# Performance work log

Hardware: AMD Instinct MI355X
Metric: run time of the kernel (lower is better)

## Reference

```python
import jax, jax.numpy as jnp
import numpy as np

N, IN_FEAT, OUT_FEAT = 16384, 1024, 4096


def setup_inputs() -> dict:
    key = jax.random.key(0)
    k_x, k_m, k_w, k_b = jax.random.split(key, 4)
    x = jax.random.normal(k_x, (N, IN_FEAT), dtype=jnp.float32)
    amask = jax.random.randint(k_m, (N,), 0, 2, dtype=jnp.int32)
    # nn.Linear(in_feat, out_feat): weight [out, in], bias [out]
    W = jax.random.normal(k_w, (OUT_FEAT, IN_FEAT), dtype=jnp.float32) * (1.0 / np.sqrt(IN_FEAT))
    b = jax.random.normal(k_b, (OUT_FEAT,), dtype=jnp.float32) * 0.001
    return {"x": x, "amask": amask, "W": W, "b": b}


def reference(x, amask, W, b):
    # Torch code gathers rows where amask != 0, applies linear (+identity act),
    # and scatters results back into a zero [N, out_feat] tensor. Equivalent
    # dense-math (jit-friendly, no data-dependent shapes): compute the linear
    # on all rows and zero out unmasked rows. Same output values.
    y = jnp.einsum('ni,oi->no', x, W) + b  # [N, out_feat]
    keep = (amask != 0)[:, None]
    return jnp.where(keep, y, jnp.zeros((), dtype=x.dtype))
```

## Files before the change

### kernel.cpp

```cpp
#include <hip/hip_runtime.h>
#include <hip/hip_bf16.h>
#include <stdint.h>

#define N_ROWS 16384
#define K_DIM  1024
#define N_OUT  4096

typedef __attribute__((ext_vector_type(8))) short short8;
typedef __attribute__((ext_vector_type(4))) float f32x4;
typedef __attribute__((ext_vector_type(4))) __bf16 bf16x4;

__global__ __launch_bounds__(1024) void scan_kernel(const int* __restrict__ amask,
                                                    int* __restrict__ idx,
                                                    int* __restrict__ zidx,
                                                    int* __restrict__ count) {
    __shared__ int sc[1024];
    const int t = threadIdx.x;
    const int base = t * 16;
    int mk[16];
#pragma unroll
    for (int g = 0; g < 4; ++g) {
        int4 m4 = reinterpret_cast<const int4*>(amask + base)[g];
        mk[g*4+0] = m4.x; mk[g*4+1] = m4.y; mk[g*4+2] = m4.z; mk[g*4+3] = m4.w;
    }
    int c = 0;
#pragma unroll
    for (int i = 0; i < 16; ++i) c += (mk[i] != 0) ? 1 : 0;
    int v = c;
    sc[t] = v;
    __syncthreads();
    for (int off = 1; off < 1024; off <<= 1) {
        int u = (t >= off) ? sc[t - off] : 0;
        __syncthreads();
        v += u; sc[t] = v;
        __syncthreads();
    }
    int b  = v - c;
    int zb = base - b;
#pragma unroll
    for (int i = 0; i < 16; ++i) {
        int r = base + i;
        if (mk[i] != 0) idx[b++] = r; else zidx[zb++] = r;
    }
    if (t == 1023) count[0] = v;
}

__global__ __launch_bounds__(256) void cvtw_gather_kernel(
    const float* __restrict__ W, const float* __restrict__ x,
    const int* __restrict__ idx, const int* __restrict__ count,
    __bf16* __restrict__ wb, __bf16* __restrict__ xb) {
    const int t = threadIdx.x;
    if (blockIdx.x < 256) {
        const int base = blockIdx.x * 4096 + t;
#pragma unroll
        for (int it = 0; it < 16; ++it) {
            const int i = base + it * 256;
            float4 v = reinterpret_cast<const float4*>(W)[i];
            bf16x4 o;
            o[0] = (__bf16)v.x; o[1] = (__bf16)v.y; o[2] = (__bf16)v.z; o[3] = (__bf16)v.w;
            reinterpret_cast<bf16x4*>(wb)[i] = o;
        }
        return;
    }
    const int cnt = count[0];
    for (int j = blockIdx.x - 256; j < cnt; j += 2048) {
        const int row = idx[j];
        float4 v = reinterpret_cast<const float4*>(x + (size_t)row * K_DIM)[t];
        bf16x4 o;
        o[0] = (__bf16)v.x; o[1] = (__bf16)v.y; o[2] = (__bf16)v.z; o[3] = (__bf16)v.w;
        reinterpret_cast<bf16x4*>(xb + (size_t)j * K_DIM)[t] = o;
    }
}


#define GLL(SRC, DSTOFF)                                                       \
    __builtin_amdgcn_global_load_lds(                                          \
        (const __attribute__((address_space(1))) void*)(SRC),                  \
        (__attribute__((address_space(3))) void*)(ldsc + (DSTOFF)), 16, 0, 0)

__global__ __launch_bounds__(256) void gemm_kernel(
    const __bf16* __restrict__ A,
    const __bf16* __restrict__ B,
    const float*  __restrict__ bias,
    const int*    __restrict__ idx,
    const int*    __restrict__ zidx,
    const int*    __restrict__ count,
    float*        __restrict__ out)
{
    __shared__ short lds_all[16384];

    const int cnt = count[0];
    const int aT  = (cnt + 127) >> 7;
    const int tn  = blockIdx.x & 31;
    const int tm  = blockIdx.x >> 5;
    const int t   = threadIdx.x;

    if (tm >= aT) {
        const int ntriv = 4096 - aT * 32;
        const int tr    = blockIdx.x - aT * 32;
        const int nz    = N_ROWS - cnt;
        const float4 zf = make_float4(0.f, 0.f, 0.f, 0.f);
        for (int i = tr; i < nz; i += ntriv) {
            const int row = zidx[i];
            float4* p = reinterpret_cast<float4*>(out + (size_t)row * N_OUT);
#pragma unroll
            for (int u = 0; u < 4; ++u)
                p[u * 256 + t] = zf;
        }
        return;
    }

    const int l  = t & 63;
    const int w  = t >> 6;
    const int wm = w >> 1;
    const int wn = w & 1;

    const int m0 = tm * 128;
    const int n0 = tn * 128;

    const int srow = t >> 3;
    const int sk   = (t & 7) * 8;
    const __bf16* pA = A + (size_t)(m0 + srow) * K_DIM + sk;
    const __bf16* pB = B + (size_t)(n0 + srow) * K_DIM + sk;
    char* ldsc = (char*)lds_all;

    const int lr  = l & 15;
    const int lqb = (l >> 4) * 16;

    f32x4 acc[4][4] = {};

    for (int k0 = 0; k0 < K_DIM; k0 += 64) {
#pragma unroll
        for (int p = 0; p < 4; ++p) {
            GLL(pA + k0 + (size_t)(p * 32) * K_DIM, p * 4096 + t * 16);
            GLL(pB + k0 + (size_t)(p * 32) * K_DIM, 16384 + p * 4096 + t * 16);
        }
        __syncthreads();

#pragma unroll
        for (int s = 0; s < 2; ++s) {
            short8 af[4], bf[4];
#pragma unroll
            for (int mi = 0; mi < 4; ++mi)
                af[mi] = *(const short8*)((char*)lds_all +
                         (wm*64 + mi*16 + lr) * 128 + s * 64 + lqb);
#pragma unroll
            for (int ni = 0; ni < 4; ++ni)
                bf[ni] = *(const short8*)((char*)lds_all + 16384 +
                         (wn*64 + ni*16 + lr) * 128 + s * 64 + lqb);

#pragma unroll
            for (int mi = 0; mi < 4; ++mi)
#pragma unroll
                for (int ni = 0; ni < 4; ++ni)
                    acc[mi][ni] = __builtin_amdgcn_mfma_f32_16x16x32_bf16(
                        af[mi], bf[ni], acc[mi][ni], 0, 0, 0);
        }
        __syncthreads();
    }

    const int lq = l >> 4;
    float bv[4];
#pragma unroll
    for (int ni = 0; ni < 4; ++ni) bv[ni] = bias[n0 + wn*64 + ni*16 + lr];

#pragma unroll
    for (int mi = 0; mi < 4; ++mi) {
        const int slot0 = m0 + wm*64 + mi*16 + lq*4;
        int rowid[4]; bool val[4];
#pragma unroll
        for (int r = 0; r < 4; ++r) {
            const int s = slot0 + r;
            val[r] = (s < cnt);
            rowid[r] = val[r] ? idx[s] : 0;
        }
#pragma unroll
        for (int ni = 0; ni < 4; ++ni) {
            const int cc = n0 + wn*64 + ni*16 + lr;
#pragma unroll
            for (int r = 0; r < 4; ++r)
                if (val[r]) out[(size_t)rowid[r] * N_OUT + cc] = acc[mi][ni][r] + bv[ni];
        }
    }
}

__global__ void naive_kernel(const float* __restrict__ x, const float* __restrict__ W,
                             const float* __restrict__ bias, const int* __restrict__ amask,
                             float* __restrict__ out) {
    int c = blockIdx.x * blockDim.x + threadIdx.x;
    int r = blockIdx.y;
    if (c >= N_OUT) return;
    if (amask[r] == 0) { out[(size_t)r * N_OUT + c] = 0.0f; return; }
    const float* xr = x + (size_t)r * K_DIM;
    const float* wr = W + (size_t)c * K_DIM;
    float s = 0.0f;
    for (int k = 0; k < K_DIM; ++k) s += xr[k] * wr[k];
    out[(size_t)r * N_OUT + c] = s + bias[c];
}

extern "C" void kernel_launch(void* const* d_in, const int* in_sizes, int n_in,
                              void* d_out, int out_size, void* d_ws, size_t ws_size,
                              hipStream_t stream) {
    const float* x     = (const float*)d_in[0];
    const int*   amask = (const int*)d_in[1];
    const float* W     = (const float*)d_in[2];
    const float* bias  = (const float*)d_in[3];
    float*       out   = (float*)d_out;

    const size_t xb_bytes = (size_t)N_ROWS * K_DIM * 2;
    const size_t wb_bytes = (size_t)N_OUT  * K_DIM * 2;
    const size_t idx_bytes = (size_t)N_ROWS * 4;
    const size_t need = xb_bytes + wb_bytes + 2 * idx_bytes + 256;

    if (ws_size < need) {
        dim3 g((N_OUT + 255) / 256, N_ROWS);
        naive_kernel<<<g, 256, 0, stream>>>(x, W, bias, amask, out);
        return;
    }

    __bf16* xb   = (__bf16*)d_ws;
    __bf16* wb   = (__bf16*)((char*)d_ws + xb_bytes);
    int*    idx  = (int*)((char*)d_ws + xb_bytes + wb_bytes);
    int*    zidx = idx + N_ROWS;
    int*    cnt  = zidx + N_ROWS;

    scan_kernel<<<1, 1024, 0, stream>>>(amask, idx, zidx, cnt);
    cvtw_gather_kernel<<<2304, 256, 0, stream>>>(W, x, idx, cnt, wb, xb);
    gemm_kernel<<<4096, 256, 0, stream>>>(xb, wb, bias, idx, zidx, cnt, out);
}
```

Baseline: 181.7 us.

## Shrink GEMM K-tile to 32 and move zero-row writes into heavy blocks

Halves the K step per iteration (64 to 32), cutting LDS use from 32KB to 16KB so more blocks can be resident per CU, at the cost of twice as many barriers and load rounds. The zero-filling of unmasked output rows is moved from the idle trailing blocks into the tail of the GEMM blocks, which now write those rows after their epilogue. Trailing blocks exit immediately unless no rows are active. This changes how the zero-store traffic overlaps with GEMM compute, and each GEMM block now carries some extra store work.

Result: faster. 153.7 us (-15.4%).

```diff
diff --git a/kernel.cpp b/kernel.cpp
--- a/kernel.cpp
+++ b/kernel.cpp
@@ -87,25 +87,25 @@
     const int*    __restrict__ count,
     float*        __restrict__ out)
 {
-    __shared__ short lds_all[16384];
+    __shared__ short lds_all[8192];
 
     const int cnt = count[0];
     const int aT  = (cnt + 127) >> 7;
     const int tn  = blockIdx.x & 31;
     const int tm  = blockIdx.x >> 5;
     const int t   = threadIdx.x;
+    const int nz  = N_ROWS - cnt;
+    const float4 zf = make_float4(0.f, 0.f, 0.f, 0.f);
 
     if (tm >= aT) {
-        const int ntriv = 4096 - aT * 32;
-        const int tr    = blockIdx.x - aT * 32;
-        const int nz    = N_ROWS - cnt;
-        const float4 zf = make_float4(0.f, 0.f, 0.f, 0.f);
-        for (int i = tr; i < nz; i += ntriv) {
-            const int row = zidx[i];
-            float4* p = reinterpret_cast<float4*>(out + (size_t)row * N_OUT);
-#pragma unroll
-            for (int u = 0; u < 4; ++u)
-                p[u * 256 + t] = zf;
+        if (aT == 0) {
+            for (int i = blockIdx.x; i < nz; i += 4096) {
+                const int row = zidx[i];
+                float4* p = reinterpret_cast<float4*>(out + (size_t)row * N_OUT);
+#pragma unroll
+                for (int u = 0; u < 4; ++u)
+                    p[u * 256 + t] = zf;
+            }
         }
         return;
     }
@@ -118,44 +118,40 @@
     const int m0 = tm * 128;
     const int n0 = tn * 128;
 
-    const int srow = t >> 3;
-    const int sk   = (t & 7) * 8;
-    const __bf16* pA = A + (size_t)(m0 + srow) * K_DIM + sk;
-    const __bf16* pB = B + (size_t)(n0 + srow) * K_DIM + sk;
+    const int srow = t >> 2;
+    const int sk8  = (t & 3) * 8;
+    const __bf16* pA0 = A + (size_t)(m0 + srow) * K_DIM + sk8;
+    const __bf16* pA1 = pA0 + (size_t)64 * K_DIM;
+    const __bf16* pB0 = B + (size_t)(n0 + srow) * K_DIM + sk8;
+    const __bf16* pB1 = pB0 + (size_t)64 * K_DIM;
     char* ldsc = (char*)lds_all;
 
-    const int lr  = l & 15;
-    const int lqb = (l >> 4) * 16;
+    const int lr = l & 15;
+    const int lk = (l >> 4) * 8;
 
     f32x4 acc[4][4] = {};
 
-    for (int k0 = 0; k0 < K_DIM; k0 += 64) {
-#pragma unroll
-        for (int p = 0; p < 4; ++p) {
-            GLL(pA + k0 + (size_t)(p * 32) * K_DIM, p * 4096 + t * 16);
-            GLL(pB + k0 + (size_t)(p * 32) * K_DIM, 16384 + p * 4096 + t * 16);
-        }
-        __syncthreads();
-
-#pragma unroll
-        for (int s = 0; s < 2; ++s) {
-            short8 af[4], bf[4];
-#pragma unroll
-            for (int mi = 0; mi < 4; ++mi)
-                af[mi] = *(const short8*)((char*)lds_all +
-                         (wm*64 + mi*16 + lr) * 128 + s * 64 + lqb);
+    for (int k0 = 0; k0 < K_DIM; k0 += 32) {
+        GLL(pA0 + k0, t * 16);
+        GLL(pA1 + k0, 4096 + t * 16);
+        GLL(pB0 + k0, 8192 + t * 16);
+        GLL(pB1 + k0, 12288 + t * 16);
+        __syncthreads();
+
+        short8 af[4], bf[4];
+#pragma unroll
+        for (int mi = 0; mi < 4; ++mi)
+            af[mi] = *(const short8*)(lds_all + (wm*64 + mi*16 + lr)*32 + lk);
+#pragma unroll
+        for (int ni = 0; ni < 4; ++ni)
+            bf[ni] = *(const short8*)(lds_all + 4096 + (wn*64 + ni*16 + lr)*32 + lk);
+
+#pragma unroll
+        for (int mi = 0; mi < 4; ++mi)
 #pragma unroll
             for (int ni = 0; ni < 4; ++ni)
-                bf[ni] = *(const short8*)((char*)lds_all + 16384 +
-                         (wn*64 + ni*16 + lr) * 128 + s * 64 + lqb);
-
-#pragma unroll
-            for (int mi = 0; mi < 4; ++mi)
-#pragma unroll
-                for (int ni = 0; ni < 4; ++ni)
-                    acc[mi][ni] = __builtin_amdgcn_mfma_f32_16x16x32_bf16(
-                        af[mi], bf[ni], acc[mi][ni], 0, 0, 0);
-        }
+                acc[mi][ni] = __builtin_amdgcn_mfma_f32_16x16x32_bf16(
+                    af[mi], bf[ni], acc[mi][ni], 0, 0, 0);
         __syncthreads();
     }
 
@@ -181,6 +177,15 @@
             for (int r = 0; r < 4; ++r)
                 if (val[r]) out[(size_t)rowid[r] * N_OUT + cc] = acc[mi][ni][r] + bv[ni];
         }
+    }
+
+    const int nheavy = aT * 32;
+    for (int i = blockIdx.x; i < nz; i += nheavy) {
+        const int row = zidx[i];
+        float4* p = reinterpret_cast<float4*>(out + (size_t)row * N_OUT);
+#pragma unroll
+        for (int u = 0; u < 4; ++u)
+            p[u * 256 + t] = zf;
     }
 }
 
```
